# Kernel tuning notes

Hardware: AMD Instinct MI355X
Metric: run time of the kernel (lower is better)

Reference implementation:

```python
import jax, jax.numpy as jnp
import numpy as np

K = 20
EPS = 1e-5  # BatchNorm eps; eval mode with running_mean=0, running_var=1


def _lrelu(x):
    return jnp.where(x >= 0, x, 0.2 * x)


def _bn(x, g, b):
    # eval-mode BN (fresh running stats: mean=0, var=1); channel axis = 1
    shape = (1, -1) + (1,) * (x.ndim - 2)
    return x * (g / jnp.sqrt(1.0 + EPS)).reshape(shape) + b.reshape(shape)


def _knn_idx(x, k):
    # x: (B, C, N). Negative squared euclidean distance, top-k = nearest.
    xx = jnp.sum(x * x, axis=1)                      # (B, N)
    inner = jnp.einsum('bcn,bcm->bnm', x, x)         # (B, N, N)
    neg_d = 2.0 * inner - xx[:, :, None] - xx[:, None, :]
    return jax.lax.top_k(neg_d, k)[1]                # (B, N, K)


def _gather(x, idx):
    # x: (B, C, N), idx: (B, N, K) -> (B, C, N, K)
    return jax.vmap(lambda xb, ib: xb[:, ib])(x, idx)


def setup_inputs() -> dict:
    key = jax.random.key(0)
    ks = jax.random.split(key, 32)
    B, N = 8, 2048
    d = {}
    d['x'] = jax.random.normal(ks[0], (B, 3, N), jnp.float32)

    def w(k_, o, i):
        return jax.random.normal(k_, (o, i), jnp.float32) * (1.0 / np.sqrt(i))

    d['W1'] = w(ks[1], 64, 3)
    d['W2'] = w(ks[2], 64, 64)
    d['W3'] = w(ks[3], 128, 64)
    d['W4'] = w(ks[4], 256, 128)
    d['W5'] = w(ks[5], 1024, 512)
    bn_dims = [64, 64, 128, 256, 1024, 512, 256]
    for i, c in enumerate(bn_dims):
        d[f'g{i+1}'] = 1.0 + 0.1 * jax.random.normal(ks[6 + 2 * i], (c,), jnp.float32)
        d[f'b{i+1}'] = 0.1 * jax.random.normal(ks[7 + 2 * i], (c,), jnp.float32)
    d['L1W'] = w(ks[20], 512, 2048)
    d['L2W'] = w(ks[21], 256, 512)
    d['L2b'] = 0.1 * jax.random.normal(ks[22], (256,), jnp.float32)
    d['L3W'] = w(ks[23], 40, 256)
    d['L3b'] = 0.1 * jax.random.normal(ks[24], (40,), jnp.float32)
    return d


def reference(x, W1, W2, W3, W4, W5,
              g1, b1, g2, b2, g3, b3, g4, b4, g5, b5, g6, b6, g7, b7,
              L1W, L2W, L2b, L3W, L3b):
    idx = _knn_idx(x, K)  # shared neighbor indices for all EdgeConv blocks

    h = _lrelu(_bn(jnp.einsum('oc,bcnk->bonk', W1, _gather(x, idx)), g1, b1))
    x1 = h.max(axis=-1)                               # (B, 64, N)
    h = _lrelu(_bn(jnp.einsum('oc,bcnk->bonk', W2, _gather(x1, idx)), g2, b2))
    x2 = h.max(axis=-1)                               # (B, 64, N)
    h = _lrelu(_bn(jnp.einsum('oc,bcnk->bonk', W3, _gather(x2, idx)), g3, b3))
    x3 = h.max(axis=-1)                               # (B, 128, N)
    h = _lrelu(_bn(jnp.einsum('oc,bcnk->bonk', W4, _gather(x3, idx)), g4, b4))
    x4 = h.max(axis=-1)                               # (B, 256, N)

    cat = jnp.concatenate([x1, x2, x3, x4], axis=1)   # (B, 512, N)
    h = _lrelu(_bn(jnp.einsum('oc,bcn->bon', W5, cat), g5, b5))  # (B, 1024, N)

    f = jnp.concatenate([h.max(axis=-1), h.mean(axis=-1)], axis=1)  # (B, 2048)
    f = _lrelu(_bn(f @ L1W.T, g6, b6))
    f = _lrelu(_bn(f @ L2W.T + L2b, g7, b7))          # dropout is identity in eval
    return f @ L3W.T + L3b                            # (B, 40)
```

## Files before the change

### kernel.cpp

```cpp
#include <hip/hip_runtime.h>
#include <math.h>


#define WS_IDX      0
#define WS_Y16      1310720
#define WS_XCAT16   9699328
#define WS_W16      26476544
#define WS_FMAX     27615232
#define WS_FSUM     27648000
#define WS_A1       27680768
#define WS_A2       27697152
#define WS_Y16B     27705344

typedef _Float16 f16x8 __attribute__((ext_vector_type(8)));
typedef float f32x4 __attribute__((ext_vector_type(4)));

struct F3 { float x, y, z; };

__device__ __forceinline__ float lrelu(float v) { return (v >= 0.f) ? v : 0.2f * v; }
__device__ __forceinline__ unsigned sortable_f32(float f) {
  unsigned b = __float_as_uint(f);
  return b ^ (((unsigned)((int)b >> 31)) | 0x80000000u);
}
__device__ __forceinline__ float desort_f32(unsigned u) {
  unsigned b = (u & 0x80000000u) ? (u ^ 0x80000000u) : ~u;
  return __uint_as_float(b);
}
__device__ __forceinline__ int xcd_swz(int i, int nwg) {
  return (i & 7) * (nwg >> 3) + (i >> 3);
}

__global__ __launch_bounds__(256) void knn_prep_kernel(
    const float* __restrict__ x, const float* __restrict__ W1,
    const float* __restrict__ g1, const float* __restrict__ b1,
    const float* __restrict__ W2, const float* __restrict__ W3,
    const float* __restrict__ W4, const float* __restrict__ W5,
    _Float16* __restrict__ w16, unsigned* __restrict__ fzero,
    int* __restrict__ idxo, _Float16* __restrict__ xcat) {
  __shared__ F3 pts_s[2048];
  __shared__ unsigned long long cand_s[8][60];
  __shared__ unsigned cnt_s[8];
  __shared__ int sel_s[8][20];
  int tid = threadIdx.x;

  if (blockIdx.x >= 2048) {
    int bid = blockIdx.x - 2048;
#pragma unroll
    for (int t = 0; t < 8; ++t) {
      int i = bid * 2048 + t * 256 + tid;
      if (i < 4096) w16[i] = (_Float16)W2[i];
      else if (i < 12288) w16[i] = (_Float16)W3[i - 4096];
      else if (i < 45056) w16[i] = (_Float16)W4[i - 12288];
      else if (i < 569344) w16[i] = (_Float16)W5[i - 45056];
      else fzero[i - 569344] = 0u;
    }
    return;
  }

  int lwave = tid >> 6, lane = tid & 63;
  int qbase = blockIdx.x * 8;
  int b = qbase >> 11;
  int nbase = qbase & 2047;
  const float* xb = x + b * 6144;
#pragma unroll
  for (int i = 0; i < 8; ++i) {
    int m = tid + i * 256;
    F3 p; p.x = xb[m]; p.y = xb[2048 + m]; p.z = xb[4096 + m];
    pts_s[m] = p;
  }
  if (lane == 0) cnt_s[lwave * 2] = 0, cnt_s[lwave * 2 + 1] = 0;
  __syncthreads();

  F3 q[2];
  float qw[2];
  unsigned keys[2][32];
  unsigned lmax[2] = {0u, 0u};
#pragma unroll
  for (int qi = 0; qi < 2; ++qi) {
    q[qi] = pts_s[nbase + lwave * 2 + qi];
    qw[qi] = q[qi].x * q[qi].x + q[qi].y * q[qi].y + q[qi].z * q[qi].z;
  }
#pragma unroll
  for (int j = 0; j < 32; ++j) {
    F3 p = pts_s[j * 64 + lane];
    float pw = p.x * p.x + p.y * p.y + p.z * p.z;
#pragma unroll
    for (int qi = 0; qi < 2; ++qi) {
      float nd = 2.0f * (q[qi].x * p.x + q[qi].y * p.y + q[qi].z * p.z) -
                 qw[qi] - pw;
      unsigned key = sortable_f32(nd);
      keys[qi][j] = key;
      lmax[qi] = (key > lmax[qi]) ? key : lmax[qi];
    }
  }
  unsigned lo[2] = {0u, 0u}, hi[2] = {0x8001u, 0x8001u};
  for (int it = 0; it < 16; ++it) {
#pragma unroll
    for (int qi = 0; qi < 2; ++qi) {
      unsigned mid = (lo[qi] + hi[qi] + 1) >> 1;
      int cnt = __popcll(__ballot(lmax[qi] >= (mid << 16)));
      if (cnt >= 20) lo[qi] = mid; else hi[qi] = mid;
    }
  }
  unsigned T[2] = {lo[0] << 16, lo[1] << 16};
#pragma unroll
  for (int j = 0; j < 32; ++j) {
    int m = j * 64 + lane;
#pragma unroll
    for (int qi = 0; qi < 2; ++qi) {
      unsigned key = keys[qi][j];
      if (key >= T[qi]) {
        unsigned pos = atomicAdd(&cnt_s[lwave * 2 + qi], 1u);
        if (pos < 60)
          cand_s[lwave * 2 + qi][pos] =
              (((unsigned long long)key) << 32) | (unsigned)(2047 - m);
      }
    }
  }
#pragma unroll
  for (int qi = 0; qi < 2; ++qi) {
    int qq = lwave * 2 + qi;
    int row = qbase + qq;
    int outb = row * 20;
    unsigned C = cnt_s[qq];
    if (C <= 60) {
      unsigned long long v = (lane < (int)C) ? ~cand_s[qq][lane] : ~0ull;
#pragma unroll
      for (int k = 2; k <= 64; k <<= 1) {
#pragma unroll
        for (int jj = k >> 1; jj > 0; jj >>= 1) {
          unsigned long long o = __shfl_xor(v, jj, 64);
          bool lower = (lane & jj) == 0;
          bool up = (lane & k) == 0;
          bool takeMin = (lower == up);
          bool sw = takeMin ? (o < v) : (o > v);
          v = sw ? o : v;
        }
      }
      if (lane < 20) {
        unsigned long long pack = ~v;
        int m = 2047 - (int)(pack & 0xFFFFFFFFu);
        idxo[outb + lane] = m;
        sel_s[qq][lane] = m;
      }
    } else {
      unsigned long long prev = ~0ull;
      for (int r = 0; r < 20; ++r) {
        unsigned long long best = 0ull;
#pragma unroll
        for (int j = 0; j < 32; ++j) {
          int m = j * 64 + lane;
          unsigned long long pk =
              (((unsigned long long)keys[qi][j]) << 32) |
              (unsigned)(2047 - m);
          bool ok = (pk < prev) & (pk > best);
          best = ok ? pk : best;
        }
#pragma unroll
        for (int off = 1; off < 64; off <<= 1) {
          unsigned long long o = __shfl_xor(best, off, 64);
          best = (o > best) ? o : best;
        }
        int m = 2047 - (int)(best & 0xFFFFFFFFu);
        if (lane == 0) { idxo[outb + r] = m; sel_s[qq][r] = m; }
        prev = best;
      }
    }
  }
  float w0 = W1[lane * 3 + 0], w1 = W1[lane * 3 + 1], w2 = W1[lane * 3 + 2];
  float inv = 1.0f / sqrtf(1.0f + 1e-5f);
  float sc = g1[lane] * inv, bi = b1[lane];
#pragma unroll
  for (int qi = 0; qi < 2; ++qi) {
    int qq = lwave * 2 + qi;
    int row = qbase + qq;
    float mx = -3.4e38f, mn = 3.4e38f;
#pragma unroll
    for (int k = 0; k < 20; ++k) {
      F3 p = pts_s[sel_s[qq][k]];
      float v = w0 * p.x + w1 * p.y + w2 * p.z;
      mx = fmaxf(mx, v);
      mn = fminf(mn, v);
    }
    float v = (sc >= 0.0f) ? mx : mn;
    xcat[row * 512 + lane] = (_Float16)lrelu(sc * v + bi);
  }
}

template <int C, int COFF>
__global__ __launch_bounds__(256) void gmax_kernel(const _Float16* __restrict__ y,
                                                   const int* __restrict__ idx,
                                                   const float* __restrict__ g,
                                                   const float* __restrict__ bb,
                                                   _Float16* __restrict__ xcat) {
  constexpr int TP = C / 8;
  int bxs = xcd_swz(blockIdx.x, gridDim.x);
  int e = bxs * 256 + threadIdx.x;
  int c8 = e & (TP - 1);
  int pg = e / TP;
  int b = pg >> 11;
  const int* ix = idx + pg * 20;
  int mm[20];
#pragma unroll
  for (int k = 0; k < 20; ++k) mm[k] = ix[k];
  int base = b * 2048 * C + c8 * 8;
  float mx[8], mn[8];
#pragma unroll
  for (int i = 0; i < 8; ++i) { mx[i] = -3.4e38f; mn[i] = 3.4e38f; }
#pragma unroll
  for (int k = 0; k < 20; ++k) {
    f16x8 v = *(const f16x8*)&y[base + mm[k] * C];
#pragma unroll
    for (int i = 0; i < 8; ++i) {
      float f = (float)v[i];
      mx[i] = fmaxf(mx[i], f);
      mn[i] = fminf(mn[i], f);
    }
  }
  float inv = 1.0f / sqrtf(1.0f + 1e-5f);
  f16x8 outv;
#pragma unroll
  for (int i = 0; i < 8; ++i) {
    float s = g[c8 * 8 + i] * inv;
    float v = (s >= 0.0f) ? mx[i] : mn[i];
    outv[i] = (_Float16)lrelu(s * v + bb[c8 * 8 + i]);
  }
  *(f16x8*)&xcat[pg * 512 + COFF + c8 * 8] = outv;
}

template <int CIN, int COUT, int XOFF>
__global__ __launch_bounds__(256) void gemm_mfma(const _Float16* __restrict__ Wh,
                                                 const _Float16* __restrict__ Xc,
                                                 _Float16* __restrict__ Y) {
  constexpr int BN = (COUT < 128) ? COUT : 128;
  constexpr int MT = (BN == 128) ? 4 : 2;
  __shared__ _Float16 Xs[128 * 40];
  __shared__ _Float16 Ws[BN * 40];
  int tid = threadIdx.x;
  int lane = tid & 63, w = tid >> 6;
  int wm = (BN == 128) ? (w & 1) : w;
  int wn = (BN == 128) ? (w >> 1) : 0;
  int col = lane & 15, quad = lane >> 4;
  int pg0 = xcd_swz(blockIdx.x, gridDim.x) * 128;
  int o0 = blockIdx.y * BN;
  int r0 = tid >> 2;
  int c8 = (tid & 3) * 8;
  f32x4 acc[MT][4] = {};
  for (int k0 = 0; k0 < CIN; k0 += 32) {
    f16x8 xa = *(const f16x8*)&Xc[(pg0 + r0) * 512 + XOFF + k0 + c8];
    f16x8 xb2 = *(const f16x8*)&Xc[(pg0 + r0 + 64) * 512 + XOFF + k0 + c8];
    f16x8 wa = *(const f16x8*)&Wh[(o0 + r0) * CIN + k0 + c8];
    f16x8 wb;
    if (BN == 128) wb = *(const f16x8*)&Wh[(o0 + r0 + 64) * CIN + k0 + c8];
    __syncthreads();
    *(f16x8*)&Xs[r0 * 40 + c8] = xa;
    *(f16x8*)&Xs[(r0 + 64) * 40 + c8] = xb2;
    *(f16x8*)&Ws[r0 * 40 + c8] = wa;
    if (BN == 128) *(f16x8*)&Ws[(r0 + 64) * 40 + c8] = wb;
    __syncthreads();
    f16x8 af[MT], bf[4];
#pragma unroll
    for (int t = 0; t < MT; ++t)
      af[t] = *(const f16x8*)&Xs[(wm * (MT * 16) + t * 16 + col) * 40 + quad * 8];
#pragma unroll
    for (int t = 0; t < 4; ++t)
      bf[t] = *(const f16x8*)&Ws[(wn * 64 + t * 16 + col) * 40 + quad * 8];
#pragma unroll
    for (int mt = 0; mt < MT; ++mt)
#pragma unroll
      for (int nt = 0; nt < 4; ++nt)
        acc[mt][nt] = __builtin_amdgcn_mfma_f32_16x16x32_f16(af[mt], bf[nt],
                                                             acc[mt][nt], 0, 0, 0);
  }
#pragma unroll
  for (int mt = 0; mt < MT; ++mt)
#pragma unroll
    for (int nt = 0; nt < 4; ++nt)
#pragma unroll
      for (int r = 0; r < 4; ++r) {
        int p = pg0 + wm * (MT * 16) + mt * 16 + quad * 4 + r;
        int ch = o0 + wn * 64 + nt * 16 + col;
        Y[p * COUT + ch] = (_Float16)acc[mt][nt][r];
      }
}

template <int CIN, int COUT, int XOFF>
__global__ __launch_bounds__(256) void gemm_gather(
    const _Float16* __restrict__ y, const int* __restrict__ idx,
    const float* __restrict__ g, const float* __restrict__ bb,
    const _Float16* __restrict__ Wh, _Float16* __restrict__ xcat,
    _Float16* __restrict__ Yout) {
  constexpr int BN = 128;
  constexpr int MT = 4;
  constexpr int CP = CIN + 8;
  __shared__ _Float16 As[128 * CP];
  __shared__ _Float16 Ws[BN * 40];
  int tid = threadIdx.x;
  int lane = tid & 63, w = tid >> 6;
  int wm = w & 1, wn = w >> 1;
  int col = lane & 15, quad = lane >> 4;
  int pg0 = xcd_swz(blockIdx.x, gridDim.x) * 128;
  int o0 = blockIdx.y * BN;
  const float inv = 1.0f / sqrtf(1.0f + 1e-5f);

  constexpr int TPR = CIN / 8;
#pragma unroll
  for (int t = 0; t < (128 * TPR) / 256; ++t) {
    int task = t * 256 + tid;
    int r = task / TPR;
    int c8 = task % TPR;
    int pg = pg0 + r;
    int b = pg >> 11;
    const int* ix = idx + pg * 20;
    int mm[20];
#pragma unroll
    for (int k = 0; k < 20; ++k) mm[k] = ix[k];
    int base = b * 2048 * CIN + c8 * 8;
    float mx[8], mn[8];
#pragma unroll
    for (int i = 0; i < 8; ++i) { mx[i] = -3.4e38f; mn[i] = 3.4e38f; }
#pragma unroll
    for (int k = 0; k < 20; ++k) {
      f16x8 v = *(const f16x8*)&y[base + mm[k] * CIN];
#pragma unroll
      for (int i = 0; i < 8; ++i) {
        float f = (float)v[i];
        mx[i] = fmaxf(mx[i], f);
        mn[i] = fminf(mn[i], f);
      }
    }
    f16x8 outv;
#pragma unroll
    for (int i = 0; i < 8; ++i) {
      float s = g[c8 * 8 + i] * inv;
      float vv = (s >= 0.0f) ? mx[i] : mn[i];
      outv[i] = (_Float16)lrelu(s * vv + bb[c8 * 8 + i]);
    }
    *(f16x8*)&As[r * CP + c8 * 8] = outv;
    if (blockIdx.y == 0) *(f16x8*)&xcat[pg * 512 + XOFF + c8 * 8] = outv;
  }
  __syncthreads();

  int r0 = tid >> 2;
  int c8b = (tid & 3) * 8;
  f32x4 acc[MT][4] = {};
  for (int k0 = 0; k0 < CIN; k0 += 32) {
    f16x8 wa = *(const f16x8*)&Wh[(o0 + r0) * CIN + k0 + c8b];
    f16x8 wb = *(const f16x8*)&Wh[(o0 + r0 + 64) * CIN + k0 + c8b];
    __syncthreads();
    *(f16x8*)&Ws[r0 * 40 + c8b] = wa;
    *(f16x8*)&Ws[(r0 + 64) * 40 + c8b] = wb;
    __syncthreads();
    f16x8 af[MT], bf[4];
#pragma unroll
    for (int t = 0; t < MT; ++t)
      af[t] = *(const f16x8*)&As[(wm * 64 + t * 16 + col) * CP + k0 + quad * 8];
#pragma unroll
    for (int t = 0; t < 4; ++t)
      bf[t] = *(const f16x8*)&Ws[(wn * 64 + t * 16 + col) * 40 + quad * 8];
#pragma unroll
    for (int mt = 0; mt < MT; ++mt)
#pragma unroll
      for (int nt = 0; nt < 4; ++nt)
        acc[mt][nt] = __builtin_amdgcn_mfma_f32_16x16x32_f16(af[mt], bf[nt],
                                                             acc[mt][nt], 0, 0, 0);
  }
#pragma unroll
  for (int mt = 0; mt < MT; ++mt)
#pragma unroll
    for (int nt = 0; nt < 4; ++nt)
#pragma unroll
      for (int r = 0; r < 4; ++r) {
        int p = pg0 + wm * 64 + mt * 16 + quad * 4 + r;
        int ch = o0 + wn * 64 + nt * 16 + col;
        Yout[p * COUT + ch] = (_Float16)acc[mt][nt][r];
      }
}

__global__ __launch_bounds__(512) void gemm_gather256(
    const _Float16* __restrict__ y, const int* __restrict__ idx,
    const float* __restrict__ g, const float* __restrict__ bb,
    const _Float16* __restrict__ Wh, _Float16* __restrict__ xcat,
    _Float16* __restrict__ Yout) {
  constexpr int CIN = 128, COUT = 256, XOFF = 128;
  constexpr int CP = CIN + 8;
  __shared__ _Float16 As[128 * CP];
  __shared__ _Float16 Ws[256 * 40];
  int tid = threadIdx.x;
  int lane = tid & 63, w = tid >> 6;
  int wm = w & 1, wn = w >> 1;
  int col = lane & 15, quad = lane >> 4;
  int pg0 = xcd_swz(blockIdx.x, gridDim.x) * 128;
  const float inv = 1.0f / sqrtf(1.0f + 1e-5f);

  constexpr int TPR = CIN / 8;
#pragma unroll
  for (int t = 0; t < (128 * TPR) / 512; ++t) {
    int task = t * 512 + tid;
    int r = task / TPR;
    int c8 = task % TPR;
    int pg = pg0 + r;
    int b = pg >> 11;
    const int* ix = idx + pg * 20;
    int mm[20];
#pragma unroll
    for (int k = 0; k < 20; ++k) mm[k] = ix[k];
    int base = b * 2048 * CIN + c8 * 8;
    float mx[8], mn[8];
#pragma unroll
    for (int i = 0; i < 8; ++i) { mx[i] = -3.4e38f; mn[i] = 3.4e38f; }
#pragma unroll
    for (int k = 0; k < 20; ++k) {
      f16x8 v = *(const f16x8*)&y[base + mm[k] * CIN];
#pragma unroll
      for (int i = 0; i < 8; ++i) {
        float f = (float)v[i];
        mx[i] = fmaxf(mx[i], f);
        mn[i] = fminf(mn[i], f);
      }
    }
    f16x8 outv;
#pragma unroll
    for (int i = 0; i < 8; ++i) {
      float s = g[c8 * 8 + i] * inv;
      float vv = (s >= 0.0f) ? mx[i] : mn[i];
      outv[i] = (_Float16)lrelu(s * vv + bb[c8 * 8 + i]);
    }
    *(f16x8*)&As[r * CP + c8 * 8] = outv;
    *(f16x8*)&xcat[pg * 512 + XOFF + c8 * 8] = outv;
  }
  __syncthreads();

  int r0 = tid >> 1;
  int c8b = (tid & 1) * 16;
  f32x4 acc[4][4] = {};
  for (int k0 = 0; k0 < CIN; k0 += 32) {
    f16x8 wa = *(const f16x8*)&Wh[r0 * CIN + k0 + c8b];
    f16x8 wb = *(const f16x8*)&Wh[r0 * CIN + k0 + c8b + 8];
    __syncthreads();
    *(f16x8*)&Ws[r0 * 40 + c8b] = wa;
    *(f16x8*)&Ws[r0 * 40 + c8b + 8] = wb;
    __syncthreads();
    f16x8 af[4], bf[4];
#pragma unroll
    for (int t = 0; t < 4; ++t)
      af[t] = *(const f16x8*)&As[(wm * 64 + t * 16 + col) * CP + k0 + quad * 8];
#pragma unroll
    for (int t = 0; t < 4; ++t)
      bf[t] = *(const f16x8*)&Ws[(wn * 64 + t * 16 + col) * 40 + quad * 8];
#pragma unroll
    for (int mt = 0; mt < 4; ++mt)
#pragma unroll
      for (int nt = 0; nt < 4; ++nt)
        acc[mt][nt] = __builtin_amdgcn_mfma_f32_16x16x32_f16(af[mt], bf[nt],
                                                             acc[mt][nt], 0, 0, 0);
  }
#pragma unroll
  for (int mt = 0; mt < 4; ++mt)
#pragma unroll
    for (int nt = 0; nt < 4; ++nt)
#pragma unroll
      for (int r = 0; r < 4; ++r) {
        int p = pg0 + wm * 64 + mt * 16 + quad * 4 + r;
        int ch = wn * 64 + nt * 16 + col;
        Yout[p * COUT + ch] = (_Float16)acc[mt][nt][r];
      }
}

typedef const __attribute__((address_space(1))) void* gas1_t;
typedef __attribute__((address_space(3))) void* las3_t;

__device__ __forceinline__ void stage16(const _Float16* g, char* l) {
  __builtin_amdgcn_global_load_lds((gas1_t)g, (las3_t)l, 16, 0, 0);
}

__global__ __launch_bounds__(512, 2) void gemm5_kernel(
    const _Float16* __restrict__ Wh, const _Float16* __restrict__ Xc,
    const float* __restrict__ g5, const float* __restrict__ b5,
    unsigned* __restrict__ fmax, float* __restrict__ fsum) {
  __shared__ __attribute__((aligned(16))) char lds[131072];
  char* ldsc = (char*)lds;
  const int tid = threadIdx.x;
  const int lane = tid & 63, w = tid >> 6;
  const int wm = w & 1, wn = w >> 1;
  const int col = lane & 15, quad = lane >> 4;
  const int pg0 = blockIdx.x * 256;
  const int o0 = blockIdx.y * 256;

  const int so = tid << 4;
  const int sl = so ^ (((so >> 9) & 3) << 5);
  const int srow0 = sl >> 7;
  const int skc0 = (sl & 127) >> 1;

#define STG(srcp, baserow, ktile, regoff, i)                                  \
  stage16((srcp) + ((baserow) + (i) * 64 + srow0) * 512 + (ktile) * 64 + skc0,\
          ldsc + (regoff) + (i) * 8192 + (w << 10))

  const int swc = ((col >> 2) & 3) << 5;
  const int labA = (col * 128 + quad * 16) ^ swc;
  const int labB = ((wn & 1) * 8192 + col * 128 + quad * 16) ^ swc;

#define RDA(m, kk) (*(const f16x8*)(rA + ((labA ^ ((kk) << 6)) + (m) * 2048)))
#define RDB(n, kk) (*(const f16x8*)(rB + ((labB ^ ((kk) << 6)) + (n) * 2048)))

  f32x4 acc[8][4] = {};

  STG(Wh, o0, 0, 32768, 0);       STG(Wh, o0, 0, 32768, 1);
  STG(Wh, o0 + 128, 0, 49152, 0); STG(Wh, o0 + 128, 0, 49152, 1);
  STG(Xc, pg0, 0, 0, 0);          STG(Xc, pg0 + 128, 0, 16384, 0);
  STG(Xc, pg0, 0, 0, 1);          STG(Xc, pg0 + 128, 0, 16384, 1);
  asm volatile("s_waitcnt vmcnt(0)" ::: "memory");
  __builtin_amdgcn_s_barrier();

  for (int t = 0; t < 8; ++t) {
    const int nt = t + 1;
    const char* rA = ldsc + (t & 1) * 65536 + wm * 16384;
    const char* rB = ldsc + (t & 1) * 65536 + 32768 + (wn >> 1) * 16384;
    const int nreg = (nt & 1) * 65536;
    f16x8 bf[4][2];
#pragma unroll
    for (int p = 0; p < 4; ++p) {
      f16x8 a[2][2];
#pragma unroll
      for (int mm = 0; mm < 2; ++mm)
#pragma unroll
        for (int kk = 0; kk < 2; ++kk)
          a[mm][kk] = RDA(2 * p + mm, kk);
      if (p == 0) {
#pragma unroll
        for (int n = 0; n < 4; ++n)
#pragma unroll
          for (int kk = 0; kk < 2; ++kk)
            bf[n][kk] = RDB(n, kk);
      }
      if (t < 7) {
        if (p == 0) { STG(Wh, o0, nt, nreg + 32768, 0);
                      STG(Wh, o0, nt, nreg + 32768, 1); }
        if (p == 1) { STG(Wh, o0 + 128, nt, nreg + 49152, 0);
                      STG(Wh, o0 + 128, nt, nreg + 49152, 1); }
        if (p == 2) { STG(Xc, pg0, nt, nreg + 0, 0);
                      STG(Xc, pg0 + 128, nt, nreg + 16384, 0); }
        if (p == 3) { STG(Xc, pg0, nt, nreg + 0, 1);
                      STG(Xc, pg0 + 128, nt, nreg + 16384, 1); }
      }
      if (p == 1) {
        if (t < 7) { asm volatile("s_waitcnt vmcnt(4)" ::: "memory"); }
        else       { asm volatile("s_waitcnt vmcnt(0)" ::: "memory"); }
      }
      if (p == 3 && t < 7) {
        asm volatile("s_waitcnt vmcnt(2)" ::: "memory");
      }
      __builtin_amdgcn_s_barrier();
      asm volatile("s_waitcnt lgkmcnt(0)" ::: "memory");
      __builtin_amdgcn_sched_barrier(0);
      __builtin_amdgcn_s_setprio(1);
#pragma unroll
      for (int mm = 0; mm < 2; ++mm)
#pragma unroll
        for (int n = 0; n < 4; ++n)
#pragma unroll
          for (int kk = 0; kk < 2; ++kk)
            acc[2 * p + mm][n] = __builtin_amdgcn_mfma_f32_16x16x32_f16(
                a[mm][kk], bf[n][kk], acc[2 * p + mm][n], 0, 0, 0);
      __builtin_amdgcn_s_setprio(0);
      __builtin_amdgcn_s_barrier();
    }
  }
#undef STG
#undef RDA
#undef RDB

  const float inv = 1.0f / sqrtf(1.0f + 1e-5f);
  const int b = pg0 >> 11;
#pragma unroll
  for (int n = 0; n < 4; ++n) {
    int ch = o0 + wn * 64 + n * 16 + col;
    float sc = g5[ch] * inv, bi = b5[ch];
    float mx = -3.4e38f, sm = 0.f;
#pragma unroll
    for (int m = 0; m < 8; ++m)
#pragma unroll
      for (int r = 0; r < 4; ++r) {
        float v = lrelu(acc[m][n][r] * sc + bi);
        mx = fmaxf(mx, v);
        sm += v;
      }
    mx = fmaxf(mx, __shfl_xor(mx, 16, 64));
    sm += __shfl_xor(sm, 16, 64);
    mx = fmaxf(mx, __shfl_xor(mx, 32, 64));
    sm += __shfl_xor(sm, 32, 64);
    if (quad == 0) {
      atomicMax(&fmax[b * 1024 + ch], sortable_f32(mx));
      atomicAdd(&fsum[b * 1024 + ch], sm);
    }
  }
}

__global__ __launch_bounds__(256) void l1_kernel(const unsigned* __restrict__ fmax,
                                                 const float* __restrict__ fsum,
                                                 const float* __restrict__ L1W,
                                                 const float* __restrict__ g6,
                                                 const float* __restrict__ b6,
                                                 float* __restrict__ a1) {
  __shared__ float red[4][8];
  int o = blockIdx.x;
  int tid = threadIdx.x, wv = tid >> 6;
  float4 w0 = *(const float4*)&L1W[o * 2048 + tid * 8];
  float4 w1 = *(const float4*)&L1W[o * 2048 + tid * 8 + 4];
  bool isMax = (tid < 128);
  float sb[8];
#pragma unroll
  for (int b = 0; b < 8; ++b) {
    float s;
    if (isMax) {
      uint4 a0 = *(const uint4*)&fmax[b * 1024 + tid * 8];
      uint4 a1v = *(const uint4*)&fmax[b * 1024 + tid * 8 + 4];
      s = desort_f32(a0.x) * w0.x + desort_f32(a0.y) * w0.y +
          desort_f32(a0.z) * w0.z + desort_f32(a0.w) * w0.w +
          desort_f32(a1v.x) * w1.x + desort_f32(a1v.y) * w1.y +
          desort_f32(a1v.z) * w1.z + desort_f32(a1v.w) * w1.w;
    } else {
      float4 f0 = *(const float4*)&fsum[b * 1024 + tid * 8 - 1024];
      float4 f1 = *(const float4*)&fsum[b * 1024 + tid * 8 - 1020];
      s = (f0.x * w0.x + f0.y * w0.y + f0.z * w0.z + f0.w * w0.w +
           f1.x * w1.x + f1.y * w1.y + f1.z * w1.z + f1.w * w1.w) *
          (1.0f / 2048.0f);
    }
    sb[b] = s;
  }
#pragma unroll
  for (int b = 0; b < 8; ++b)
#pragma unroll
    for (int off = 1; off < 64; off <<= 1) sb[b] += __shfl_xor(sb[b], off, 64);
  if ((tid & 63) == 0) {
#pragma unroll
    for (int b = 0; b < 8; ++b) red[wv][b] = sb[b];
  }
  __syncthreads();
  if (tid < 8) {
    float s = red[0][tid] + red[1][tid] + red[2][tid] + red[3][tid];
    float scv = g6[o] / sqrtf(1.0f + 1e-5f);
    a1[tid * 512 + o] = lrelu(s * scv + b6[o]);
  }
}

__global__ __launch_bounds__(256) void l2_kernel(const float* __restrict__ a1,
                                                 const float* __restrict__ L2W,
                                                 const float* __restrict__ L2b,
                                                 const float* __restrict__ g7,
                                                 const float* __restrict__ b7,
                                                 float* __restrict__ a2) {
  int gw = (blockIdx.x * 256 + threadIdx.x) >> 6;
  int lane = threadIdx.x & 63;
  int b = gw >> 8, o = gw & 255;
  float s = 0.f;
#pragma unroll
  for (int i = 0; i < 8; ++i) {
    int j = lane + i * 64;
    s += a1[b * 512 + j] * L2W[o * 512 + j];
  }
#pragma unroll
  for (int off = 1; off < 64; off <<= 1) s += __shfl_xor(s, off, 64);
  if (lane == 0) {
    float v = s + L2b[o];
    float scv = g7[o] / sqrtf(1.0f + 1e-5f);
    a2[b * 256 + o] = lrelu(v * scv + b7[o]);
  }
}

__global__ __launch_bounds__(256) void l3_kernel(const float* __restrict__ a2,
                                                 const float* __restrict__ L3W,
                                                 const float* __restrict__ L3b,
                                                 float* __restrict__ out) {
  int gw = (blockIdx.x * 256 + threadIdx.x) >> 6;
  int lane = threadIdx.x & 63;
  int b = gw / 40, o = gw % 40;
  float s = 0.f;
#pragma unroll
  for (int i = 0; i < 4; ++i) {
    int j = lane + i * 64;
    s += a2[b * 256 + j] * L3W[o * 256 + j];
  }
#pragma unroll
  for (int off = 1; off < 64; off <<= 1) s += __shfl_xor(s, off, 64);
  if (lane == 0) out[b * 40 + o] = s + L3b[o];
}

extern "C" void kernel_launch(void* const* d_in, const int* in_sizes, int n_in,
                              void* d_out, int out_size, void* d_ws, size_t ws_size,
                              hipStream_t stream) {
  const float* x = (const float*)d_in[0];
  const float* W1 = (const float*)d_in[1];
  const float* W2 = (const float*)d_in[2];
  const float* W3 = (const float*)d_in[3];
  const float* W4 = (const float*)d_in[4];
  const float* W5 = (const float*)d_in[5];
  const float* g1 = (const float*)d_in[6];  const float* b1 = (const float*)d_in[7];
  const float* g2 = (const float*)d_in[8];  const float* b2 = (const float*)d_in[9];
  const float* g3 = (const float*)d_in[10]; const float* b3 = (const float*)d_in[11];
  const float* g4 = (const float*)d_in[12]; const float* b4 = (const float*)d_in[13];
  const float* g5 = (const float*)d_in[14]; const float* b5 = (const float*)d_in[15];
  const float* g6 = (const float*)d_in[16]; const float* b6 = (const float*)d_in[17];
  const float* g7 = (const float*)d_in[18]; const float* b7 = (const float*)d_in[19];
  const float* L1W = (const float*)d_in[20];
  const float* L2W = (const float*)d_in[21];
  const float* L2b = (const float*)d_in[22];
  const float* L3W = (const float*)d_in[23];
  const float* L3b = (const float*)d_in[24];

  char* w = (char*)d_ws;
  int* idxb = (int*)(w + WS_IDX);
  _Float16* y16 = (_Float16*)(w + WS_Y16);
  _Float16* y16b = (_Float16*)(w + WS_Y16B);
  _Float16* xcat16 = (_Float16*)(w + WS_XCAT16);
  _Float16* w16 = (_Float16*)(w + WS_W16);
  unsigned* fmax = (unsigned*)(w + WS_FMAX);
  float* fsum = (float*)(w + WS_FSUM);
  float* a1 = (float*)(w + WS_A1);
  float* a2 = (float*)(w + WS_A2);

  knn_prep_kernel<<<2334, 256, 0, stream>>>(x, W1, g1, b1, W2, W3, W4, W5,
                                            w16, fmax, idxb, xcat16);
  gemm_mfma<64, 64, 0><<<dim3(128, 1), 256, 0, stream>>>(w16, xcat16, y16);
  gemm_gather<64, 128, 64><<<dim3(128, 1), 256, 0, stream>>>(
      y16, idxb, g2, b2, w16 + 4096, xcat16, y16b);
  gemm_gather256<<<dim3(128, 1), 512, 0, stream>>>(
      y16b, idxb, g3, b3, w16 + 12288, xcat16, y16);
  gmax_kernel<256, 256><<<2048, 256, 0, stream>>>(y16, idxb, g4, b4, xcat16);
  gemm5_kernel<<<dim3(64, 4), 512, 0, stream>>>(w16 + 45056, xcat16, g5, b5, fmax, fsum);
  l1_kernel<<<512, 256, 0, stream>>>(fmax, fsum, L1W, g6, b6, a1);
  l2_kernel<<<512, 256, 0, stream>>>(a1, L2W, L2b, g7, b7, a2);
  l3_kernel<<<80, 256, 0, stream>>>(a2, L3W, L3b, (float*)d_out);
}
```

Measured before the change: 211.9 us.

## Use one wave per kNN query and ballot-based candidate compaction

Each kNN block now runs 512 threads, one wave per query, where before each wave handled two queries. Points are staged into shared memory once per eight queries using more threads, and the weight-conversion blocks are resized to match. Candidate compaction now uses a ballot plus prefix popcount in place of shared-memory atomics, which removes the counter array and the atomic traffic. Register pressure per wave drops (32 keys instead of 64), which could raise occupancy, but the 512-thread blocks may limit how many blocks fit per CU.

```diff
diff --git a/kernel.cpp b/kernel.cpp
--- a/kernel.cpp
+++ b/kernel.cpp
@@ -30,7 +30,7 @@
   return (i & 7) * (nwg >> 3) + (i >> 3);
 }
 
-__global__ __launch_bounds__(256) void knn_prep_kernel(
+__global__ __launch_bounds__(512) void knn_prep_kernel(
     const float* __restrict__ x, const float* __restrict__ W1,
     const float* __restrict__ g1, const float* __restrict__ b1,
     const float* __restrict__ W2, const float* __restrict__ W3,
@@ -39,7 +39,6 @@
     int* __restrict__ idxo, _Float16* __restrict__ xcat) {
   __shared__ F3 pts_s[2048];
   __shared__ unsigned long long cand_s[8][60];
-  __shared__ unsigned cnt_s[8];
   __shared__ int sel_s[8][20];
   int tid = threadIdx.x;
 
@@ -47,7 +46,7 @@
     int bid = blockIdx.x - 2048;
 #pragma unroll
     for (int t = 0; t < 8; ++t) {
-      int i = bid * 2048 + t * 256 + tid;
+      int i = bid * 4096 + t * 512 + tid;
       if (i < 4096) w16[i] = (_Float16)W2[i];
       else if (i < 12288) w16[i] = (_Float16)W3[i - 4096];
       else if (i < 45056) w16[i] = (_Float16)W4[i - 12288];
@@ -57,127 +56,109 @@
     return;
   }
 
-  int lwave = tid >> 6, lane = tid & 63;
+  int wv = tid >> 6, lane = tid & 63;
   int qbase = blockIdx.x * 8;
   int b = qbase >> 11;
   int nbase = qbase & 2047;
   const float* xb = x + b * 6144;
 #pragma unroll
-  for (int i = 0; i < 8; ++i) {
-    int m = tid + i * 256;
+  for (int i = 0; i < 4; ++i) {
+    int m = tid + i * 512;
     F3 p; p.x = xb[m]; p.y = xb[2048 + m]; p.z = xb[4096 + m];
     pts_s[m] = p;
   }
-  if (lane == 0) cnt_s[lwave * 2] = 0, cnt_s[lwave * 2 + 1] = 0;
   __syncthreads();
 
-  F3 q[2];
-  float qw[2];
-  unsigned keys[2][32];
-  unsigned lmax[2] = {0u, 0u};
-#pragma unroll
-  for (int qi = 0; qi < 2; ++qi) {
-    q[qi] = pts_s[nbase + lwave * 2 + qi];
-    qw[qi] = q[qi].x * q[qi].x + q[qi].y * q[qi].y + q[qi].z * q[qi].z;
-  }
+  F3 q = pts_s[nbase + wv];
+  float qw = q.x * q.x + q.y * q.y + q.z * q.z;
+  unsigned keys[32];
+  unsigned lmax = 0u;
 #pragma unroll
   for (int j = 0; j < 32; ++j) {
     F3 p = pts_s[j * 64 + lane];
     float pw = p.x * p.x + p.y * p.y + p.z * p.z;
-#pragma unroll
-    for (int qi = 0; qi < 2; ++qi) {
-      float nd = 2.0f * (q[qi].x * p.x + q[qi].y * p.y + q[qi].z * p.z) -
-                 qw[qi] - pw;
-      unsigned key = sortable_f32(nd);
-      keys[qi][j] = key;
-      lmax[qi] = (key > lmax[qi]) ? key : lmax[qi];
-    }
-  }
-  unsigned lo[2] = {0u, 0u}, hi[2] = {0x8001u, 0x8001u};
+    float nd = 2.0f * (q.x * p.x + q.y * p.y + q.z * p.z) - qw - pw;
+    unsigned key = sortable_f32(nd);
+    keys[j] = key;
+    lmax = (key > lmax) ? key : lmax;
+  }
+  unsigned lo = 0u, hi = 0x8001u;
   for (int it = 0; it < 16; ++it) {
-#pragma unroll
-    for (int qi = 0; qi < 2; ++qi) {
-      unsigned mid = (lo[qi] + hi[qi] + 1) >> 1;
-      int cnt = __popcll(__ballot(lmax[qi] >= (mid << 16)));
-      if (cnt >= 20) lo[qi] = mid; else hi[qi] = mid;
-    }
-  }
-  unsigned T[2] = {lo[0] << 16, lo[1] << 16};
+    unsigned mid = (lo + hi + 1) >> 1;
+    int cnt = __popcll(__ballot(lmax >= (mid << 16)));
+    if (cnt >= 20) lo = mid; else hi = mid;
+  }
+  unsigned T = lo << 16;
+  unsigned cnt = 0u;
+  unsigned long long below = (1ull << lane) - 1ull;
 #pragma unroll
   for (int j = 0; j < 32; ++j) {
     int m = j * 64 + lane;
-#pragma unroll
-    for (int qi = 0; qi < 2; ++qi) {
-      unsigned key = keys[qi][j];
-      if (key >= T[qi]) {
-        unsigned pos = atomicAdd(&cnt_s[lwave * 2 + qi], 1u);
-        if (pos < 60)
-          cand_s[lwave * 2 + qi][pos] =
-              (((unsigned long long)key) << 32) | (unsigned)(2047 - m);
-      }
-    }
-  }
-#pragma unroll
-  for (int qi = 0; qi < 2; ++qi) {
-    int qq = lwave * 2 + qi;
-    int row = qbase + qq;
-    int outb = row * 20;
-    unsigned C = cnt_s[qq];
-    if (C <= 60) {
-      unsigned long long v = (lane < (int)C) ? ~cand_s[qq][lane] : ~0ull;
-#pragma unroll
-      for (int k = 2; k <= 64; k <<= 1) {
-#pragma unroll
-        for (int jj = k >> 1; jj > 0; jj >>= 1) {
-          unsigned long long o = __shfl_xor(v, jj, 64);
-          bool lower = (lane & jj) == 0;
-          bool up = (lane & k) == 0;
-          bool takeMin = (lower == up);
-          bool sw = takeMin ? (o < v) : (o > v);
-          v = sw ? o : v;
-        }
-      }
-      if (lane < 20) {
-        unsigned long long pack = ~v;
-        int m = 2047 - (int)(pack & 0xFFFFFFFFu);
-        idxo[outb + lane] = m;
-        sel_s[qq][lane] = m;
-      }
-    } else {
-      unsigned long long prev = ~0ull;
-      for (int r = 0; r < 20; ++r) {
-        unsigned long long best = 0ull;
-#pragma unroll
-        for (int j = 0; j < 32; ++j) {
-          int m = j * 64 + lane;
-          unsigned long long pk =
-              (((unsigned long long)keys[qi][j]) << 32) |
-              (unsigned)(2047 - m);
-          bool ok = (pk < prev) & (pk > best);
-          best = ok ? pk : best;
-        }
-#pragma unroll
-        for (int off = 1; off < 64; off <<= 1) {
-          unsigned long long o = __shfl_xor(best, off, 64);
-          best = (o > best) ? o : best;
-        }
-        int m = 2047 - (int)(best & 0xFFFFFFFFu);
-        if (lane == 0) { idxo[outb + r] = m; sel_s[qq][r] = m; }
-        prev = best;
-      }
-    }
-  }
+    bool pass = keys[j] >= T;
+    unsigned long long mask = __ballot(pass);
+    if (pass) {
+      unsigned pos = cnt + (unsigned)__popcll(mask & below);
+      if (pos < 60)
+        cand_s[wv][pos] =
+            (((unsigned long long)keys[j]) << 32) | (unsigned)(2047 - m);
+    }
+    cnt += (unsigned)__popcll(mask);
+  }
+
+  int row = qbase + wv;
+  int outb = row * 20;
+  unsigned C = cnt;
+  if (C <= 60) {
+    unsigned long long v = (lane < (int)C) ? ~cand_s[wv][lane] : ~0ull;
+#pragma unroll
+    for (int k = 2; k <= 64; k <<= 1) {
+#pragma unroll
+      for (int jj = k >> 1; jj > 0; jj >>= 1) {
+        unsigned long long o = __shfl_xor(v, jj, 64);
+        bool lower = (lane & jj) == 0;
+        bool up = (lane & k) == 0;
+        bool takeMin = (lower == up);
+        bool sw = takeMin ? (o < v) : (o > v);
+        v = sw ? o : v;
+      }
+    }
+    if (lane < 20) {
+      unsigned long long pack = ~v;
+      int m = 2047 - (int)(pack & 0xFFFFFFFFu);
+      idxo[outb + lane] = m;
+      sel_s[wv][lane] = m;
+    }
+  } else {
+    unsigned long long prev = ~0ull;
+    for (int r = 0; r < 20; ++r) {
+      unsigned long long best = 0ull;
+#pragma unroll
+      for (int j = 0; j < 32; ++j) {
+        int m = j * 64 + lane;
+        unsigned long long pk =
+            (((unsigned long long)keys[j]) << 32) | (unsigned)(2047 - m);
+        bool ok = (pk < prev) & (pk > best);
+        best = ok ? pk : best;
+      }
+#pragma unroll
+      for (int off = 1; off < 64; off <<= 1) {
+        unsigned long long o = __shfl_xor(best, off, 64);
+        best = (o > best) ? o : best;
+      }
+      int m = 2047 - (int)(best & 0xFFFFFFFFu);
+      if (lane == 0) { idxo[outb + r] = m; sel_s[wv][r] = m; }
+      prev = best;
+    }
+  }
+
   float w0 = W1[lane * 3 + 0], w1 = W1[lane * 3 + 1], w2 = W1[lane * 3 + 2];
   float inv = 1.0f / sqrtf(1.0f + 1e-5f);
   float sc = g1[lane] * inv, bi = b1[lane];
-#pragma unroll
-  for (int qi = 0; qi < 2; ++qi) {
-    int qq = lwave * 2 + qi;
-    int row = qbase + qq;
+  {
     float mx = -3.4e38f, mn = 3.4e38f;
 #pragma unroll
     for (int k = 0; k < 20; ++k) {
-      F3 p = pts_s[sel_s[qq][k]];
+      F3 p = pts_s[sel_s[wv][k]];
       float v = w0 * p.x + w1 * p.y + w2 * p.z;
       mx = fmaxf(mx, v);
       mn = fminf(mn, v);
@@ -719,7 +700,7 @@
   float* a1 = (float*)(w + WS_A1);
   float* a2 = (float*)(w + WS_A2);
 
-  knn_prep_kernel<<<2334, 256, 0, stream>>>(x, W1, g1, b1, W2, W3, W4, W5,
+  knn_prep_kernel<<<2191, 512, 0, stream>>>(x, W1, g1, b1, W2, W3, W4, W5,
                                             w16, fmax, idxb, xcat16);
   gemm_mfma<64, 64, 0><<<dim3(128, 1), 256, 0, stream>>>(w16, xcat16, y16);
   gemm_gather<64, 128, 64><<<dim3(128, 1), 256, 0, stream>>>(
```

New measurement: 204.1 us. -3.7%, faster.
